# Kernel tuning notes

Hardware: AMD Instinct MI355X
Metric: run time of the kernel (lower is better)

## Reference

```python
import jax, jax.numpy as jnp
import numpy as np
import math

N, E, B, T = 100000, 500000, 4096, 12
IN, HID, H = 64, 32, 4
HC = HID * H  # 128
ED = 4


def setup_inputs() -> dict:
    key = jax.random.key(0)
    ks = jax.random.split(key, 40)
    w = lambda k, shape: jax.random.normal(k, shape, jnp.float32) * 0.05
    inp = {
        'x': jax.random.normal(ks[0], (N, IN), jnp.float32),
        'edge_index': jax.random.randint(ks[1], (2, E), 0, N, jnp.int32),
        'edge_attr': jax.random.normal(ks[2], (E, ED), jnp.float32),
        'batch': jnp.sort(jax.random.randint(ks[3], (N,), 0, B, jnp.int32)),
        'r_target': jax.random.randint(ks[4], (B,), 0, T, jnp.int32),
        # layer 1 (in=IN)
        'Wq1': w(ks[5], (IN, HC)), 'bq1': w(ks[6], (HC,)),
        'Wk1': w(ks[7], (IN, HC)), 'bk1': w(ks[8], (HC,)),
        'Wv1': w(ks[9], (IN, HC)), 'bv1': w(ks[10], (HC,)),
        'We1': w(ks[11], (ED, HC)),
        'Ws1': w(ks[12], (IN, HC)), 'bs1': w(ks[13], (HC,)),
        # layers 2 and 3 stacked (in=HC)
        'Wq23': w(ks[14], (2, HC, HC)), 'bq23': w(ks[15], (2, HC)),
        'Wk23': w(ks[16], (2, HC, HC)), 'bk23': w(ks[17], (2, HC)),
        'Wv23': w(ks[18], (2, HC, HC)), 'bv23': w(ks[19], (2, HC)),
        'We23': w(ks[20], (2, ED, HC)),
        'Ws23': w(ks[21], (2, HC, HC)), 'bs23': w(ks[22], (2, HC)),
        # per-task linear heads (out_channels=1)
        'head_W': w(ks[23], (T, HC)), 'head_b': w(ks[24], (T,)),
    }
    return inp


def tconv(x, src, dst, ea, Wq, bq, Wk, bk, Wv, bv, We, Ws, bs):
    """PyG TransformerConv: gather -> per-edge MHA score -> segment softmax -> scatter."""
    q = (x @ Wq + bq).reshape(-1, H, HID)   # [N,H,C]
    k = (x @ Wk + bk).reshape(-1, H, HID)
    v = (x @ Wv + bv).reshape(-1, H, HID)
    e = (ea @ We).reshape(-1, H, HID)       # [E,H,C] (lin_edge has no bias)
    kj = k[src] + e                          # [E,H,C]
    alpha = (q[dst] * kj).sum(-1) / math.sqrt(HID)          # [E,H]
    amax = jax.ops.segment_max(alpha, dst, num_segments=N)  # [N,H]
    alpha = jnp.exp(alpha - amax[dst])
    asum = jax.ops.segment_sum(alpha, dst, num_segments=N)
    alpha = alpha / (asum[dst] + 1e-16)
    msg = (v[src] + e) * alpha[..., None]                   # [E,H,C]
    out = jax.ops.segment_sum(msg, dst, num_segments=N).reshape(N, HC)
    return out + x @ Ws + bs                 # root_weight skip connection


def reference(x, edge_index, edge_attr, batch, r_target,
              Wq1, bq1, Wk1, bk1, Wv1, bv1, We1, Ws1, bs1,
              Wq23, bq23, Wk23, bk23, Wv23, bv23, We23, Ws23, bs23,
              head_W, head_b):
    src, dst = edge_index[0], edge_index[1]
    h = jax.nn.relu(tconv(x, src, dst, edge_attr, Wq1, bq1, Wk1, bk1, Wv1, bv1, We1, Ws1, bs1))
    h = jax.nn.relu(tconv(h, src, dst, edge_attr, Wq23[0], bq23[0], Wk23[0], bk23[0], Wv23[0], bv23[0], We23[0], Ws23[0], bs23[0]))
    h = tconv(h, src, dst, edge_attr, Wq23[1], bq23[1], Wk23[1], bk23[1], Wv23[1], bv23[1], We23[1], Ws23[1], bs23[1])
    # global mean pool per graph
    cnt = jax.ops.segment_sum(jnp.ones((N,), h.dtype), batch, num_segments=B)
    pooled = jax.ops.segment_sum(h, batch, num_segments=B) / jnp.maximum(cnt, 1.0)[:, None]  # [B,HC]
    # dropout p=0.3 is a no-op in eval mode
    # per-task head selected by r_target (out_channels=1, squeezed)
    return (pooled * head_W[r_target]).sum(-1) + head_b[r_target]  # [B]
```

## Files before the change

### kernel.cpp

```cpp
#include <hip/hip_runtime.h>
#include <hip/hip_bf16.h>

#define NN 100000
#define EE 500000
#define BB 4096
#define HC 128
#define SCAN_ELEM 1024
#define NSB ((NN + SCAN_ELEM - 1) / SCAN_ELEM)

typedef __bf16 bf16_t;
typedef bf16_t bf16x8 __attribute__((ext_vector_type(8)));
typedef float f32x4 __attribute__((ext_vector_type(4)));
typedef float f32x2 __attribute__((ext_vector_type(2)));

__device__ __forceinline__ unsigned short f2bf(float f) {
    unsigned u = __builtin_bit_cast(unsigned, f);
    u += 0x7FFFu + ((u >> 16) & 1u);
    return (unsigned short)(u >> 16);
}
__device__ __forceinline__ float bflo(unsigned u) {
    return __builtin_bit_cast(float, u << 16);
}
__device__ __forceinline__ float bfhi(unsigned u) {
    return __builtin_bit_cast(float, u & 0xFFFF0000u);
}
__device__ __forceinline__ f32x2 unpk2(unsigned u) {
    return (f32x2){ bflo(u), bfhi(u) };
}

__global__ __launch_bounds__(256) void prep_w(
    const float* __restrict__ Wq, const float* __restrict__ Wk,
    const float* __restrict__ Wv, const float* __restrict__ Ws,
    unsigned short* __restrict__ Wt, int K)
{
    const int g = blockIdx.x * 256 + threadIdx.x;
    const int per = K * 128;
    if (g >= 4 * per) return;
    const int p = g / per, r = g - p * per;
    const int k = r >> 7, n = r & 127;
    const float* W = p == 0 ? Wq : p == 1 ? Wk : p == 2 ? Wv : Ws;
    Wt[(size_t)p * per + (size_t)n * K + k] = f2bf(W[k * 128 + n]);
}

template<int NKT, int F32A>
__global__ __launch_bounds__(256) void gemm_mfma(
    const unsigned short* __restrict__ Abf,
    const float* __restrict__ xf,
    const unsigned short* __restrict__ Wt,
    const float* __restrict__ bq, const float* __restrict__ bk,
    const float* __restrict__ bv, const float* __restrict__ bs,
    unsigned* __restrict__ QSb, unsigned* __restrict__ KVb)
{
    constexpr int K = NKT * 32;
    const int lane = threadIdx.x & 63;
    const int p = threadIdx.x >> 6;
    const int m = lane & 15, kq = lane >> 4;
    const int rows0 = blockIdx.x * 32;

    const unsigned short* Wp = Wt + (size_t)p * 128 * K;
    const float* bias = p == 0 ? bq : p == 1 ? bk : p == 2 ? bv : bs;

    bf16x8 a[2][NKT];
#pragma unroll
    for (int mt = 0; mt < 2; mt++)
#pragma unroll
        for (int kt = 0; kt < NKT; kt++) {
            if constexpr (F32A) {
                const float* pr = xf + (size_t)(rows0 + mt * 16 + m) * K + kt * 32 + kq * 8;
                const float4 f0 = *(const float4*)pr;
                const float4 f1 = *(const float4*)(pr + 4);
                union { bf16x8 v; unsigned short u8[8]; } cv;
                cv.u8[0] = f2bf(f0.x); cv.u8[1] = f2bf(f0.y);
                cv.u8[2] = f2bf(f0.z); cv.u8[3] = f2bf(f0.w);
                cv.u8[4] = f2bf(f1.x); cv.u8[5] = f2bf(f1.y);
                cv.u8[6] = f2bf(f1.z); cv.u8[7] = f2bf(f1.w);
                a[mt][kt] = cv.v;
            } else {
                a[mt][kt] = *(const bf16x8*)(Abf + (size_t)(rows0 + mt * 16 + m) * K + kt * 32 + kq * 8);
            }
        }

    f32x4 acc[2][8];
#pragma unroll
    for (int mt = 0; mt < 2; mt++)
#pragma unroll
        for (int nt = 0; nt < 8; nt++)
            acc[mt][nt] = (f32x4){0.f, 0.f, 0.f, 0.f};

#pragma unroll
    for (int nt = 0; nt < 8; nt++) {
#pragma unroll
        for (int kt = 0; kt < NKT; kt++) {
            const bf16x8 b = *(const bf16x8*)(Wp + (size_t)(nt * 16 + m) * K + kt * 32 + kq * 8);
            acc[0][nt] = __builtin_amdgcn_mfma_f32_16x16x32_bf16(a[0][kt], b, acc[0][nt], 0, 0, 0);
            acc[1][nt] = __builtin_amdgcn_mfma_f32_16x16x32_bf16(a[1][kt], b, acc[1][nt], 0, 0, 0);
        }
    }

    unsigned* out = p == 0 ? QSb : p == 1 ? KVb : p == 2 ? (KVb + 64) : (QSb + 64);
#pragma unroll
    for (int nt = 0; nt < 8; nt++) {
        const float bi = bias[nt * 16 + m];
#pragma unroll
        for (int mt = 0; mt < 2; mt++) {
#pragma unroll
            for (int r = 0; r < 4; r++) {
                const float v0 = acc[mt][nt][r] + bi;
                const float v1 = __shfl_xor(v0, 1);
                if (!(m & 1)) {
                    const unsigned pk = (unsigned)f2bf(v0) | ((unsigned)f2bf(v1) << 16);
                    out[(size_t)(rows0 + mt * 16 + kq * 4 + r) * 128 + nt * 8 + (m >> 1)] = pk;
                }
            }
        }
    }
}

__global__ __launch_bounds__(256) void deg_k(const int* __restrict__ ei, int* __restrict__ deg)
{
    const int e = blockIdx.x * 256 + threadIdx.x;
    if (e < EE) atomicAdd(&deg[ei[EE + e]], 1);
}

__global__ __launch_bounds__(256) void scan_part(const int* __restrict__ deg,
                                                 int* __restrict__ bsum)
{
    __shared__ int red[256];
    const int base = blockIdx.x * SCAN_ELEM + threadIdx.x * 4;
    int s = 0;
#pragma unroll
    for (int j = 0; j < 4; j++) { const int i = base + j; if (i < NN) s += deg[i]; }
    red[threadIdx.x] = s;
    __syncthreads();
    for (int st = 128; st > 0; st >>= 1) {
        if (threadIdx.x < st) red[threadIdx.x] += red[threadIdx.x + st];
        __syncthreads();
    }
    if (threadIdx.x == 0) bsum[blockIdx.x] = red[0];
}

__global__ __launch_bounds__(128) void scan_top(const int* __restrict__ bsum,
                                                int* __restrict__ boff)
{
    __shared__ int buf[128];
    const int v = (threadIdx.x < NSB) ? bsum[threadIdx.x] : 0;
    buf[threadIdx.x] = v;
    __syncthreads();
    for (int s = 1; s < 128; s <<= 1) {
        const int t = (threadIdx.x >= s) ? buf[threadIdx.x - s] : 0;
        __syncthreads();
        buf[threadIdx.x] += t;
        __syncthreads();
    }
    if (threadIdx.x < NSB) boff[threadIdx.x] = buf[threadIdx.x] - v;
}

__global__ __launch_bounds__(256) void scan_final(const int* __restrict__ deg,
                                                  const int* __restrict__ boff,
                                                  int* __restrict__ off,
                                                  int* __restrict__ cursor)
{
    __shared__ int tsum[256];
    const int base = blockIdx.x * SCAN_ELEM + threadIdx.x * 4;
    int vals[4];
    int s = 0;
#pragma unroll
    for (int j = 0; j < 4; j++) {
        const int i = base + j;
        vals[j] = (i < NN) ? deg[i] : 0;
        s += vals[j];
    }
    tsum[threadIdx.x] = s;
    __syncthreads();
    for (int st = 1; st < 256; st <<= 1) {
        const int t = (threadIdx.x >= st) ? tsum[threadIdx.x - st] : 0;
        __syncthreads();
        tsum[threadIdx.x] += t;
        __syncthreads();
    }
    int ex = boff[blockIdx.x] + tsum[threadIdx.x] - s;
#pragma unroll
    for (int j = 0; j < 4; j++) {
        const int i = base + j;
        if (i < NN) { off[i] = ex; cursor[i] = ex; }
        ex += vals[j];
    }
    if (blockIdx.x == NSB - 1 && threadIdx.x == 255)
        off[NN] = boff[blockIdx.x] + tsum[255];
}

__global__ __launch_bounds__(256) void bucket_k(const int* __restrict__ ei,
                                                const float* __restrict__ ea,
                                                int* __restrict__ cursor,
                                                int* __restrict__ esrc,
                                                float4* __restrict__ eaf)
{
    const int e = blockIdx.x * 256 + threadIdx.x;
    if (e < EE) {
        const int d = ei[EE + e];
        const int p = atomicAdd(&cursor[d], 1);
        esrc[p] = ei[e];
        eaf[p] = *(const float4*)(ea + (size_t)e * 4);
    }
}

__global__ __launch_bounds__(256) void cnt_k(const int* __restrict__ batch,
                                             float* __restrict__ cnt)
{
    const int n = blockIdx.x * 256 + threadIdx.x;
    if (n < NN) atomicAdd(&cnt[batch[n]], 1.0f);
}

__global__ __launch_bounds__(256) void edge_fused(
    const int* __restrict__ esrc, const float4* __restrict__ eaf,
    const float* __restrict__ We,
    const unsigned* __restrict__ QSb, const unsigned* __restrict__ KVb,
    const int* __restrict__ off,
    unsigned short* __restrict__ Hb,
    const int* __restrict__ batch, float* __restrict__ pooled,
    int fuse_pool)
{
    const int lane = threadIdx.x & 63;
    const int slot = lane >> 4;
    const int c8   = lane & 15;
    const int cb   = c8 * 8;
    const int ceq  = cb + slot * 2;
    const int n = blockIdx.x * 4 + (threadIdx.x >> 6);

    const int beg = off[n], end = off[n + 1];

    const uint4 qv = *(const uint4*)(QSb + (size_t)n * 128 + c8 * 4);
    const unsigned sku = QSb[(size_t)n * 128 + 64 + c8 * 4 + slot];
    f32x2 q2[4];
    q2[0] = unpk2(qv.x); q2[1] = unpk2(qv.y);
    q2[2] = unpk2(qv.z); q2[3] = unpk2(qv.w);

    float qep[4];
#pragma unroll
    for (int d = 0; d < 4; d++) {
        const float4 wa = *(const float4*)(We + d * HC + cb);
        const float4 wb = *(const float4*)(We + d * HC + cb + 4);
        qep[d] = wa.x * q2[0].x + wa.y * q2[0].y + wa.z * q2[1].x + wa.w * q2[1].y
               + wb.x * q2[2].x + wb.y * q2[2].y + wb.z * q2[3].x + wb.w * q2[3].y;
    }

    f32x2 num2[4] = {(f32x2){0.f, 0.f}, (f32x2){0.f, 0.f},
                     (f32x2){0.f, 0.f}, (f32x2){0.f, 0.f}};
    f32x4 s4 = (f32x4){0.f, 0.f, 0.f, 0.f};
    float den = 0.f;

    if (beg < end) {
        const int e1 = end - 1;
        int p0 = beg + slot; if (p0 > e1) p0 = e1;
        int src = esrc[p0];
        float4 a4 = eaf[p0];
        for (int base = beg; base < end; base += 4) {
            const unsigned* kv = KVb + (size_t)src * 128 + c8 * 4;
            const uint4 ku = *(const uint4*)kv;
            const uint4 vu = *(const uint4*)(kv + 64);
            const float4 ac = a4;
            const bool act = (base + slot) < end;
            if (base + 4 < end) {
                int pn = base + 4 + slot; if (pn > e1) pn = e1;
                src = esrc[pn]; a4 = eaf[pn];
            }
            f32x2 t2 = q2[0] * unpk2(ku.x);
            t2 += q2[1] * unpk2(ku.y);
            t2 += q2[2] * unpk2(ku.z);
            t2 += q2[3] * unpk2(ku.w);
            float tot = t2.x + t2.y
                      + ac.x * qep[0] + ac.y * qep[1] + ac.z * qep[2] + ac.w * qep[3];
            tot += __shfl_xor(tot, 1);
            tot += __shfl_xor(tot, 2);
            float al = __expf(tot * 0.17677669529663687f);
            if (!act) al = 0.f;
            num2[0] += unpk2(vu.x) * al;
            num2[1] += unpk2(vu.y) * al;
            num2[2] += unpk2(vu.z) * al;
            num2[3] += unpk2(vu.w) * al;
            s4.x += ac.x * al; s4.y += ac.y * al;
            s4.z += ac.z * al; s4.w += ac.w * al;
            den += al;
        }
    }

#pragma unroll
    for (int j = 0; j < 4; j++) {
        num2[j].x += __shfl_xor(num2[j].x, 16);
        num2[j].y += __shfl_xor(num2[j].y, 16);
        num2[j].x += __shfl_xor(num2[j].x, 32);
        num2[j].y += __shfl_xor(num2[j].y, 32);
    }
    s4.x += __shfl_xor(s4.x, 16); s4.y += __shfl_xor(s4.y, 16);
    s4.z += __shfl_xor(s4.z, 16); s4.w += __shfl_xor(s4.w, 16);
    s4.x += __shfl_xor(s4.x, 32); s4.y += __shfl_xor(s4.y, 32);
    s4.z += __shfl_xor(s4.z, 32); s4.w += __shfl_xor(s4.w, 32);
    den += __shfl_xor(den, 16);
    den += __shfl_xor(den, 32);
    const float inv = 1.f / (den + 1e-16f);

    f32x2 mynum = slot == 0 ? num2[0] : slot == 1 ? num2[1]
                : slot == 2 ? num2[2] : num2[3];
    float ev0 = 0.f, ev1 = 0.f;
#pragma unroll
    for (int d = 0; d < 4; d++) {
        const float2 wd = *(const float2*)(We + d * HC + ceq);
        const float sd = d == 0 ? s4.x : d == 1 ? s4.y : d == 2 ? s4.z : s4.w;
        ev0 += sd * wd.x;
        ev1 += sd * wd.y;
    }
    const float o0 = (mynum.x + ev0) * inv + bflo(sku);
    const float o1 = (mynum.y + ev1) * inv + bfhi(sku);

    if (!fuse_pool) {
        const float r0 = fmaxf(o0, 0.f), r1 = fmaxf(o1, 0.f);
        const unsigned pk = (unsigned)f2bf(r0) | ((unsigned)f2bf(r1) << 16);
        *(unsigned*)(Hb + (size_t)n * HC + ceq) = pk;
    } else {
        const int b = batch[n];
        atomicAdd(pooled + (size_t)b * HC + ceq,     o0);
        atomicAdd(pooled + (size_t)b * HC + ceq + 1, o1);
    }
}

__global__ __launch_bounds__(256) void head_k(
    const float* __restrict__ pooled, const float* __restrict__ cnt,
    const int* __restrict__ rt, const float* __restrict__ hW,
    const float* __restrict__ hb, float* __restrict__ out)
{
    const int lane = threadIdx.x & 63;
    const int b = blockIdx.x * 4 + (threadIdx.x >> 6);
    if (b >= BB) return;
    const int t = rt[b];
    const int c = lane * 2;
    const float2 p2 = *(const float2*)(pooled + (size_t)b * HC + c);
    const float2 w2 = *(const float2*)(hW + (size_t)t * HC + c);
    float part = p2.x * w2.x + p2.y * w2.y;
    part += __shfl_xor(part, 1);
    part += __shfl_xor(part, 2);
    part += __shfl_xor(part, 4);
    part += __shfl_xor(part, 8);
    part += __shfl_xor(part, 16);
    part += __shfl_xor(part, 32);
    if (lane == 0) out[b] = part / fmaxf(cnt[b], 1.0f) + hb[t];
}

extern "C" void kernel_launch(void* const* d_in, const int* in_sizes, int n_in,
                              void* d_out, int out_size, void* d_ws, size_t ws_size,
                              hipStream_t stream) {
    const float* x      = (const float*)d_in[0];
    const int*   ei     = (const int*)d_in[1];
    const float* ea     = (const float*)d_in[2];
    const int*   batch  = (const int*)d_in[3];
    const int*   rt     = (const int*)d_in[4];

    unsigned* QSb = (unsigned*)d_ws;
    unsigned* KVb = QSb + 12800000;
    unsigned short* Abf = (unsigned short*)(KVb + 12800000);
    float4* eaf   = (float4*)(Abf + 12800000);
    unsigned short* Wt = (unsigned short*)(eaf + 500000);
    float* pooled = (float*)(Wt + 65536);
    float* cnt    = pooled + 524288;
    int*   esrc   = (int*)(cnt + 4096);
    int*   deg    = esrc + 500000;
    int*   off    = deg + 100000;
    int*   cursor = off + 100004;
    int*   bsum   = cursor + 100000;
    int*   boff   = bsum + 128;

    hipMemsetAsync(deg, 0, 100000 * sizeof(int), stream);
    deg_k<<<(EE + 255) / 256, 256, 0, stream>>>(ei, deg);
    scan_part<<<NSB, 256, 0, stream>>>(deg, bsum);
    scan_top<<<1, 128, 0, stream>>>(bsum, boff);
    scan_final<<<NSB, 256, 0, stream>>>(deg, boff, off, cursor);
    bucket_k<<<(EE + 255) / 256, 256, 0, stream>>>(ei, ea, cursor, esrc, eaf);

    hipMemsetAsync(pooled, 0, (size_t)(BB * HC + BB) * sizeof(float), stream);
    cnt_k<<<(NN + 255) / 256, 256, 0, stream>>>(batch, cnt);

    for (int l = 0; l < 3; l++) {
        const int K = (l == 0) ? 64 : 128;
        const float *Wq, *Wk, *Wv, *Wsk, *bq, *bk, *bv, *bs, *We;
        if (l == 0) {
            Wq = (const float*)d_in[5];  bq = (const float*)d_in[6];
            Wk = (const float*)d_in[7];  bk = (const float*)d_in[8];
            Wv = (const float*)d_in[9];  bv = (const float*)d_in[10];
            We = (const float*)d_in[11];
            Wsk= (const float*)d_in[12]; bs = (const float*)d_in[13];
        } else {
            const int j = l - 1;
            Wq = (const float*)d_in[14] + (size_t)j * HC * HC;  bq = (const float*)d_in[15] + j * HC;
            Wk = (const float*)d_in[16] + (size_t)j * HC * HC;  bk = (const float*)d_in[17] + j * HC;
            Wv = (const float*)d_in[18] + (size_t)j * HC * HC;  bv = (const float*)d_in[19] + j * HC;
            We = (const float*)d_in[20] + (size_t)j * 4 * HC;
            Wsk= (const float*)d_in[21] + (size_t)j * HC * HC;  bs = (const float*)d_in[22] + j * HC;
        }

        prep_w<<<(4 * K * 128 + 255) / 256, 256, 0, stream>>>(Wq, Wk, Wv, Wsk, Wt, K);
        if (K == 64)
            gemm_mfma<2, 1><<<NN / 32, 256, 0, stream>>>(Abf, x, Wt, bq, bk, bv, bs, QSb, KVb);
        else
            gemm_mfma<4, 0><<<NN / 32, 256, 0, stream>>>(Abf, x, Wt, bq, bk, bv, bs, QSb, KVb);
        edge_fused<<<NN / 4, 256, 0, stream>>>(esrc, eaf, We, QSb, KVb, off,
                                               Abf, batch, pooled,
                                               l == 2 ? 1 : 0);
    }

    head_k<<<BB / 4, 256, 0, stream>>>(pooled, cnt, rt,
        (const float*)d_in[23], (const float*)d_in[24], (float*)d_out);
}
```

Before: 664.6 us.

## Process eight edges per wave iteration with sixteen channels per lane

Remaps the per-node wave so each lane covers 16 channels (two heads' worth across a lane pair) and 8 edge slots run concurrently instead of 4. This halves the loop trip count per node and issues more independent gathers in flight, which targets latency on low-degree nodes (average degree is about 5). In exchange it doubles per-lane registers for q, num and loaded K/V, makes the cross-slot reduction longer (three shuffle stages over more values), and leaves more slots idle on nodes with few edges.

```diff
diff --git a/kernel.cpp b/kernel.cpp
--- a/kernel.cpp
+++ b/kernel.cpp
@@ -221,31 +221,39 @@
     int fuse_pool)
 {
     const int lane = threadIdx.x & 63;
-    const int slot = lane >> 4;
-    const int c8   = lane & 15;
-    const int cb   = c8 * 8;
+    const int slot = lane >> 3;
+    const int c8   = lane & 7;
+    const int cb   = c8 * 16;
     const int ceq  = cb + slot * 2;
     const int n = blockIdx.x * 4 + (threadIdx.x >> 6);
 
-    const int beg = off[n], end = off[n + 1];
-
-    const uint4 qv = *(const uint4*)(QSb + (size_t)n * 128 + c8 * 4);
-    const unsigned sku = QSb[(size_t)n * 128 + 64 + c8 * 4 + slot];
-    f32x2 q2[4];
-    q2[0] = unpk2(qv.x); q2[1] = unpk2(qv.y);
-    q2[2] = unpk2(qv.z); q2[3] = unpk2(qv.w);
+    const int2 be = *(const int2*)(off + n);
+    const int beg = be.x, end = be.y;
+
+    const uint4 qva = *(const uint4*)(QSb + (size_t)n * 128 + c8 * 8);
+    const uint4 qvb = *(const uint4*)(QSb + (size_t)n * 128 + c8 * 8 + 4);
+    const unsigned sku = QSb[(size_t)n * 128 + 64 + c8 * 8 + slot];
+    f32x2 q2[8];
+    q2[0] = unpk2(qva.x); q2[1] = unpk2(qva.y);
+    q2[2] = unpk2(qva.z); q2[3] = unpk2(qva.w);
+    q2[4] = unpk2(qvb.x); q2[5] = unpk2(qvb.y);
+    q2[6] = unpk2(qvb.z); q2[7] = unpk2(qvb.w);
 
     float qep[4];
 #pragma unroll
     for (int d = 0; d < 4; d++) {
-        const float4 wa = *(const float4*)(We + d * HC + cb);
-        const float4 wb = *(const float4*)(We + d * HC + cb + 4);
-        qep[d] = wa.x * q2[0].x + wa.y * q2[0].y + wa.z * q2[1].x + wa.w * q2[1].y
-               + wb.x * q2[2].x + wb.y * q2[2].y + wb.z * q2[3].x + wb.w * q2[3].y;
-    }
-
-    f32x2 num2[4] = {(f32x2){0.f, 0.f}, (f32x2){0.f, 0.f},
-                     (f32x2){0.f, 0.f}, (f32x2){0.f, 0.f}};
+        float acc = 0.f;
+#pragma unroll
+        for (int j = 0; j < 4; j++) {
+            const float4 w4 = *(const float4*)(We + d * HC + cb + j * 4);
+            acc += w4.x * q2[2 * j].x + w4.y * q2[2 * j].y
+                 + w4.z * q2[2 * j + 1].x + w4.w * q2[2 * j + 1].y;
+        }
+        qep[d] = acc;
+    }
+
+    f32x2 num2[8] = {(f32x2){0.f,0.f},(f32x2){0.f,0.f},(f32x2){0.f,0.f},(f32x2){0.f,0.f},
+                     (f32x2){0.f,0.f},(f32x2){0.f,0.f},(f32x2){0.f,0.f},(f32x2){0.f,0.f}};
     f32x4 s4 = (f32x4){0.f, 0.f, 0.f, 0.f};
     float den = 0.f;
 
@@ -254,30 +262,39 @@
         int p0 = beg + slot; if (p0 > e1) p0 = e1;
         int src = esrc[p0];
         float4 a4 = eaf[p0];
-        for (int base = beg; base < end; base += 4) {
-            const unsigned* kv = KVb + (size_t)src * 128 + c8 * 4;
-            const uint4 ku = *(const uint4*)kv;
-            const uint4 vu = *(const uint4*)(kv + 64);
+        for (int base = beg; base < end; base += 8) {
+            const unsigned* kv = KVb + (size_t)src * 128 + c8 * 8;
+            const uint4 ka = *(const uint4*)kv;
+            const uint4 kb = *(const uint4*)(kv + 4);
+            const uint4 va = *(const uint4*)(kv + 64);
+            const uint4 vb = *(const uint4*)(kv + 68);
             const float4 ac = a4;
             const bool act = (base + slot) < end;
-            if (base + 4 < end) {
-                int pn = base + 4 + slot; if (pn > e1) pn = e1;
+            if (base + 8 < end) {
+                int pn = base + 8 + slot; if (pn > e1) pn = e1;
                 src = esrc[pn]; a4 = eaf[pn];
             }
-            f32x2 t2 = q2[0] * unpk2(ku.x);
-            t2 += q2[1] * unpk2(ku.y);
-            t2 += q2[2] * unpk2(ku.z);
-            t2 += q2[3] * unpk2(ku.w);
+            f32x2 t2 = q2[0] * unpk2(ka.x);
+            t2 += q2[1] * unpk2(ka.y);
+            t2 += q2[2] * unpk2(ka.z);
+            t2 += q2[3] * unpk2(ka.w);
+            t2 += q2[4] * unpk2(kb.x);
+            t2 += q2[5] * unpk2(kb.y);
+            t2 += q2[6] * unpk2(kb.z);
+            t2 += q2[7] * unpk2(kb.w);
             float tot = t2.x + t2.y
                       + ac.x * qep[0] + ac.y * qep[1] + ac.z * qep[2] + ac.w * qep[3];
             tot += __shfl_xor(tot, 1);
-            tot += __shfl_xor(tot, 2);
             float al = __expf(tot * 0.17677669529663687f);
             if (!act) al = 0.f;
-            num2[0] += unpk2(vu.x) * al;
-            num2[1] += unpk2(vu.y) * al;
-            num2[2] += unpk2(vu.z) * al;
-            num2[3] += unpk2(vu.w) * al;
+            num2[0] += unpk2(va.x) * al;
+            num2[1] += unpk2(va.y) * al;
+            num2[2] += unpk2(va.z) * al;
+            num2[3] += unpk2(va.w) * al;
+            num2[4] += unpk2(vb.x) * al;
+            num2[5] += unpk2(vb.y) * al;
+            num2[6] += unpk2(vb.z) * al;
+            num2[7] += unpk2(vb.w) * al;
             s4.x += ac.x * al; s4.y += ac.y * al;
             s4.z += ac.z * al; s4.w += ac.w * al;
             den += al;
@@ -285,22 +302,29 @@
     }
 
 #pragma unroll
-    for (int j = 0; j < 4; j++) {
-        num2[j].x += __shfl_xor(num2[j].x, 16);
-        num2[j].y += __shfl_xor(num2[j].y, 16);
-        num2[j].x += __shfl_xor(num2[j].x, 32);
-        num2[j].y += __shfl_xor(num2[j].y, 32);
-    }
-    s4.x += __shfl_xor(s4.x, 16); s4.y += __shfl_xor(s4.y, 16);
-    s4.z += __shfl_xor(s4.z, 16); s4.w += __shfl_xor(s4.w, 16);
-    s4.x += __shfl_xor(s4.x, 32); s4.y += __shfl_xor(s4.y, 32);
-    s4.z += __shfl_xor(s4.z, 32); s4.w += __shfl_xor(s4.w, 32);
-    den += __shfl_xor(den, 16);
-    den += __shfl_xor(den, 32);
+    for (int st = 8; st < 64; st <<= 1) {
+#pragma unroll
+        for (int j = 0; j < 8; j++) {
+            num2[j].x += __shfl_xor(num2[j].x, st);
+            num2[j].y += __shfl_xor(num2[j].y, st);
+        }
+        s4.x += __shfl_xor(s4.x, st); s4.y += __shfl_xor(s4.y, st);
+        s4.z += __shfl_xor(s4.z, st); s4.w += __shfl_xor(s4.w, st);
+        den += __shfl_xor(den, st);
+    }
     const float inv = 1.f / (den + 1e-16f);
 
-    f32x2 mynum = slot == 0 ? num2[0] : slot == 1 ? num2[1]
-                : slot == 2 ? num2[2] : num2[3];
+    f32x2 mynum;
+    switch (slot) {
+        case 0: mynum = num2[0]; break;
+        case 1: mynum = num2[1]; break;
+        case 2: mynum = num2[2]; break;
+        case 3: mynum = num2[3]; break;
+        case 4: mynum = num2[4]; break;
+        case 5: mynum = num2[5]; break;
+        case 6: mynum = num2[6]; break;
+        default: mynum = num2[7]; break;
+    }
     float ev0 = 0.f, ev1 = 0.f;
 #pragma unroll
     for (int d = 0; d < 4; d++) {
```

After: 899.6 us. +35.4%, slower.

## Process two destination nodes per wavefront in edge kernel, fold cnt into scan

Applied to the files above, without the earlier changes.

The edge attention kernel now assigns two adjacent destination nodes to each 64-lane wavefront and interleaves their gathers and softmax accumulation. This halves the grid and aims to expose more independent memory loads per wave, hiding the latency of random K/V gathers. The separate graph-count kernel is removed and its atomics are folded into scan_final, saving one launch. The cost is higher register pressure and some divergence when the two nodes have different degrees.

```diff
diff --git a/kernel.cpp b/kernel.cpp
--- a/kernel.cpp
+++ b/kernel.cpp
@@ -158,7 +158,9 @@
 __global__ __launch_bounds__(256) void scan_final(const int* __restrict__ deg,
                                                   const int* __restrict__ boff,
                                                   int* __restrict__ off,
-                                                  int* __restrict__ cursor)
+                                                  int* __restrict__ cursor,
+                                                  const int* __restrict__ batch,
+                                                  float* __restrict__ cnt)
 {
     __shared__ int tsum[256];
     const int base = blockIdx.x * SCAN_ELEM + threadIdx.x * 4;
@@ -182,7 +184,10 @@
 #pragma unroll
     for (int j = 0; j < 4; j++) {
         const int i = base + j;
-        if (i < NN) { off[i] = ex; cursor[i] = ex; }
+        if (i < NN) {
+            off[i] = ex; cursor[i] = ex;
+            atomicAdd(&cnt[batch[i]], 1.0f);
+        }
         ex += vals[j];
     }
     if (blockIdx.x == NSB - 1 && threadIdx.x == 255)
@@ -202,13 +207,6 @@
         esrc[p] = ei[e];
         eaf[p] = *(const float4*)(ea + (size_t)e * 4);
     }
-}
-
-__global__ __launch_bounds__(256) void cnt_k(const int* __restrict__ batch,
-                                             float* __restrict__ cnt)
-{
-    const int n = blockIdx.x * 256 + threadIdx.x;
-    if (n < NN) atomicAdd(&cnt[batch[n]], 1.0f);
 }
 
 __global__ __launch_bounds__(256) void edge_fused(
@@ -225,101 +223,162 @@
     const int c8   = lane & 15;
     const int cb   = c8 * 8;
     const int ceq  = cb + slot * 2;
-    const int n = blockIdx.x * 4 + (threadIdx.x >> 6);
-
-    const int beg = off[n], end = off[n + 1];
-
-    const uint4 qv = *(const uint4*)(QSb + (size_t)n * 128 + c8 * 4);
-    const unsigned sku = QSb[(size_t)n * 128 + 64 + c8 * 4 + slot];
-    f32x2 q2[4];
-    q2[0] = unpk2(qv.x); q2[1] = unpk2(qv.y);
-    q2[2] = unpk2(qv.z); q2[3] = unpk2(qv.w);
-
-    float qep[4];
+    const int nA = (blockIdx.x * 4 + (threadIdx.x >> 6)) * 2;
+    const int nB = nA + 1;
+
+    const int2 beA = *(const int2*)(off + nA);
+    const int begA = beA.x, endA = beA.y;
+    const int begB = endA, endB = off[nB + 1];
+    const int dA = endA - begA, dB = endB - begB;
+
+    const uint4 qvA = *(const uint4*)(QSb + (size_t)nA * 128 + c8 * 4);
+    const uint4 qvB = *(const uint4*)(QSb + (size_t)nB * 128 + c8 * 4);
+    const unsigned skA = QSb[(size_t)nA * 128 + 64 + c8 * 4 + slot];
+    const unsigned skB = QSb[(size_t)nB * 128 + 64 + c8 * 4 + slot];
+    f32x2 qA[4], qB[4];
+    qA[0] = unpk2(qvA.x); qA[1] = unpk2(qvA.y);
+    qA[2] = unpk2(qvA.z); qA[3] = unpk2(qvA.w);
+    qB[0] = unpk2(qvB.x); qB[1] = unpk2(qvB.y);
+    qB[2] = unpk2(qvB.z); qB[3] = unpk2(qvB.w);
+
+    float qepA[4], qepB[4];
 #pragma unroll
     for (int d = 0; d < 4; d++) {
         const float4 wa = *(const float4*)(We + d * HC + cb);
         const float4 wb = *(const float4*)(We + d * HC + cb + 4);
-        qep[d] = wa.x * q2[0].x + wa.y * q2[0].y + wa.z * q2[1].x + wa.w * q2[1].y
-               + wb.x * q2[2].x + wb.y * q2[2].y + wb.z * q2[3].x + wb.w * q2[3].y;
-    }
-
-    f32x2 num2[4] = {(f32x2){0.f, 0.f}, (f32x2){0.f, 0.f},
-                     (f32x2){0.f, 0.f}, (f32x2){0.f, 0.f}};
-    f32x4 s4 = (f32x4){0.f, 0.f, 0.f, 0.f};
-    float den = 0.f;
-
-    if (beg < end) {
-        const int e1 = end - 1;
-        int p0 = beg + slot; if (p0 > e1) p0 = e1;
-        int src = esrc[p0];
-        float4 a4 = eaf[p0];
-        for (int base = beg; base < end; base += 4) {
-            const unsigned* kv = KVb + (size_t)src * 128 + c8 * 4;
-            const uint4 ku = *(const uint4*)kv;
-            const uint4 vu = *(const uint4*)(kv + 64);
-            const float4 ac = a4;
-            const bool act = (base + slot) < end;
-            if (base + 4 < end) {
-                int pn = base + 4 + slot; if (pn > e1) pn = e1;
-                src = esrc[pn]; a4 = eaf[pn];
+        qepA[d] = wa.x * qA[0].x + wa.y * qA[0].y + wa.z * qA[1].x + wa.w * qA[1].y
+                + wb.x * qA[2].x + wb.y * qA[2].y + wb.z * qA[3].x + wb.w * qA[3].y;
+        qepB[d] = wa.x * qB[0].x + wa.y * qB[0].y + wa.z * qB[1].x + wa.w * qB[1].y
+                + wb.x * qB[2].x + wb.y * qB[2].y + wb.z * qB[3].x + wb.w * qB[3].y;
+    }
+
+    f32x2 numA[4] = {(f32x2){0.f,0.f},(f32x2){0.f,0.f},(f32x2){0.f,0.f},(f32x2){0.f,0.f}};
+    f32x2 numB[4] = {(f32x2){0.f,0.f},(f32x2){0.f,0.f},(f32x2){0.f,0.f},(f32x2){0.f,0.f}};
+    f32x4 s4A = (f32x4){0.f,0.f,0.f,0.f}, s4B = (f32x4){0.f,0.f,0.f,0.f};
+    float denA = 0.f, denB = 0.f;
+
+    int srcA = 0, srcB = 0;
+    float4 a4A = make_float4(0.f,0.f,0.f,0.f), a4B = make_float4(0.f,0.f,0.f,0.f);
+    if (dA > 0) { const int p = begA + (slot < dA ? slot : dA - 1); srcA = esrc[p]; a4A = eaf[p]; }
+    if (dB > 0) { const int p = begB + (slot < dB ? slot : dB - 1); srcB = esrc[p]; a4B = eaf[p]; }
+
+    const int dmax = dA > dB ? dA : dB;
+    for (int o = 0; o < dmax; o += 4) {
+        const bool anyA = o < dA, anyB = o < dB;
+        uint4 kuA, vuA, kuB, vuB;
+        float4 acA, acB;
+        if (anyA) {
+            const unsigned* kv = KVb + (size_t)srcA * 128 + c8 * 4;
+            kuA = *(const uint4*)kv; vuA = *(const uint4*)(kv + 64);
+        }
+        if (anyB) {
+            const unsigned* kv = KVb + (size_t)srcB * 128 + c8 * 4;
+            kuB = *(const uint4*)kv; vuB = *(const uint4*)(kv + 64);
+        }
+        if (anyA) {
+            acA = a4A;
+            if (o + 4 < dA) {
+                const int t = o + 4 + slot;
+                const int p = begA + (t < dA ? t : dA - 1);
+                srcA = esrc[p]; a4A = eaf[p];
             }
-            f32x2 t2 = q2[0] * unpk2(ku.x);
-            t2 += q2[1] * unpk2(ku.y);
-            t2 += q2[2] * unpk2(ku.z);
-            t2 += q2[3] * unpk2(ku.w);
+        }
+        if (anyB) {
+            acB = a4B;
+            if (o + 4 < dB) {
+                const int t = o + 4 + slot;
+                const int p = begB + (t < dB ? t : dB - 1);
+                srcB = esrc[p]; a4B = eaf[p];
+            }
+        }
+        if (anyA) {
+            f32x2 t2 = qA[0] * unpk2(kuA.x);
+            t2 += qA[1] * unpk2(kuA.y);
+            t2 += qA[2] * unpk2(kuA.z);
+            t2 += qA[3] * unpk2(kuA.w);
             float tot = t2.x + t2.y
-                      + ac.x * qep[0] + ac.y * qep[1] + ac.z * qep[2] + ac.w * qep[3];
+                      + acA.x * qepA[0] + acA.y * qepA[1] + acA.z * qepA[2] + acA.w * qepA[3];
             tot += __shfl_xor(tot, 1);
             tot += __shfl_xor(tot, 2);
             float al = __expf(tot * 0.17677669529663687f);
-            if (!act) al = 0.f;
-            num2[0] += unpk2(vu.x) * al;
-            num2[1] += unpk2(vu.y) * al;
-            num2[2] += unpk2(vu.z) * al;
-            num2[3] += unpk2(vu.w) * al;
-            s4.x += ac.x * al; s4.y += ac.y * al;
-            s4.z += ac.z * al; s4.w += ac.w * al;
-            den += al;
-        }
-    }
-
-#pragma unroll
-    for (int j = 0; j < 4; j++) {
-        num2[j].x += __shfl_xor(num2[j].x, 16);
-        num2[j].y += __shfl_xor(num2[j].y, 16);
-        num2[j].x += __shfl_xor(num2[j].x, 32);
-        num2[j].y += __shfl_xor(num2[j].y, 32);
-    }
-    s4.x += __shfl_xor(s4.x, 16); s4.y += __shfl_xor(s4.y, 16);
-    s4.z += __shfl_xor(s4.z, 16); s4.w += __shfl_xor(s4.w, 16);
-    s4.x += __shfl_xor(s4.x, 32); s4.y += __shfl_xor(s4.y, 32);
-    s4.z += __shfl_xor(s4.z, 32); s4.w += __shfl_xor(s4.w, 32);
-    den += __shfl_xor(den, 16);
-    den += __shfl_xor(den, 32);
-    const float inv = 1.f / (den + 1e-16f);
-
-    f32x2 mynum = slot == 0 ? num2[0] : slot == 1 ? num2[1]
-                : slot == 2 ? num2[2] : num2[3];
-    float ev0 = 0.f, ev1 = 0.f;
+            if ((o + slot) >= dA) al = 0.f;
+            numA[0] += unpk2(vuA.x) * al;
+            numA[1] += unpk2(vuA.y) * al;
+            numA[2] += unpk2(vuA.z) * al;
+            numA[3] += unpk2(vuA.w) * al;
+            s4A.x += acA.x * al; s4A.y += acA.y * al;
+            s4A.z += acA.z * al; s4A.w += acA.w * al;
+            denA += al;
+        }
+        if (anyB) {
+            f32x2 t2 = qB[0] * unpk2(kuB.x);
+            t2 += qB[1] * unpk2(kuB.y);
+            t2 += qB[2] * unpk2(kuB.z);
+            t2 += qB[3] * unpk2(kuB.w);
+            float tot = t2.x + t2.y
+                      + acB.x * qepB[0] + acB.y * qepB[1] + acB.z * qepB[2] + acB.w * qepB[3];
+            tot += __shfl_xor(tot, 1);
+            tot += __shfl_xor(tot, 2);
+            float al = __expf(tot * 0.17677669529663687f);
+            if ((o + slot) >= dB) al = 0.f;
+            numB[0] += unpk2(vuB.x) * al;
+            numB[1] += unpk2(vuB.y) * al;
+            numB[2] += unpk2(vuB.z) * al;
+            numB[3] += unpk2(vuB.w) * al;
+            s4B.x += acB.x * al; s4B.y += acB.y * al;
+            s4B.z += acB.z * al; s4B.w += acB.w * al;
+            denB += al;
+        }
+    }
+
+#pragma unroll
+    for (int st = 16; st < 64; st <<= 1) {
+#pragma unroll
+        for (int j = 0; j < 4; j++) {
+            numA[j].x += __shfl_xor(numA[j].x, st);
+            numA[j].y += __shfl_xor(numA[j].y, st);
+            numB[j].x += __shfl_xor(numB[j].x, st);
+            numB[j].y += __shfl_xor(numB[j].y, st);
+        }
+        s4A.x += __shfl_xor(s4A.x, st); s4A.y += __shfl_xor(s4A.y, st);
+        s4A.z += __shfl_xor(s4A.z, st); s4A.w += __shfl_xor(s4A.w, st);
+        s4B.x += __shfl_xor(s4B.x, st); s4B.y += __shfl_xor(s4B.y, st);
+        s4B.z += __shfl_xor(s4B.z, st); s4B.w += __shfl_xor(s4B.w, st);
+        denA += __shfl_xor(denA, st);
+        denB += __shfl_xor(denB, st);
+    }
+    const float invA = 1.f / (denA + 1e-16f);
+    const float invB = 1.f / (denB + 1e-16f);
+
+    f32x2 mynA = slot == 0 ? numA[0] : slot == 1 ? numA[1]
+               : slot == 2 ? numA[2] : numA[3];
+    f32x2 mynB = slot == 0 ? numB[0] : slot == 1 ? numB[1]
+               : slot == 2 ? numB[2] : numB[3];
+    float evA0 = 0.f, evA1 = 0.f, evB0 = 0.f, evB1 = 0.f;
 #pragma unroll
     for (int d = 0; d < 4; d++) {
         const float2 wd = *(const float2*)(We + d * HC + ceq);
-        const float sd = d == 0 ? s4.x : d == 1 ? s4.y : d == 2 ? s4.z : s4.w;
-        ev0 += sd * wd.x;
-        ev1 += sd * wd.y;
-    }
-    const float o0 = (mynum.x + ev0) * inv + bflo(sku);
-    const float o1 = (mynum.y + ev1) * inv + bfhi(sku);
+        const float sdA = d == 0 ? s4A.x : d == 1 ? s4A.y : d == 2 ? s4A.z : s4A.w;
+        const float sdB = d == 0 ? s4B.x : d == 1 ? s4B.y : d == 2 ? s4B.z : s4B.w;
+        evA0 += sdA * wd.x; evA1 += sdA * wd.y;
+        evB0 += sdB * wd.x; evB1 += sdB * wd.y;
+    }
+    const float oA0 = (mynA.x + evA0) * invA + bflo(skA);
+    const float oA1 = (mynA.y + evA1) * invA + bfhi(skA);
+    const float oB0 = (mynB.x + evB0) * invB + bflo(skB);
+    const float oB1 = (mynB.y + evB1) * invB + bfhi(skB);
 
     if (!fuse_pool) {
-        const float r0 = fmaxf(o0, 0.f), r1 = fmaxf(o1, 0.f);
-        const unsigned pk = (unsigned)f2bf(r0) | ((unsigned)f2bf(r1) << 16);
-        *(unsigned*)(Hb + (size_t)n * HC + ceq) = pk;
+        const unsigned pkA = (unsigned)f2bf(fmaxf(oA0, 0.f)) | ((unsigned)f2bf(fmaxf(oA1, 0.f)) << 16);
+        const unsigned pkB = (unsigned)f2bf(fmaxf(oB0, 0.f)) | ((unsigned)f2bf(fmaxf(oB1, 0.f)) << 16);
+        *(unsigned*)(Hb + (size_t)nA * HC + ceq) = pkA;
+        *(unsigned*)(Hb + (size_t)nB * HC + ceq) = pkB;
     } else {
-        const int b = batch[n];
-        atomicAdd(pooled + (size_t)b * HC + ceq,     o0);
-        atomicAdd(pooled + (size_t)b * HC + ceq + 1, o1);
+        const int bA = batch[nA], bB = batch[nB];
+        atomicAdd(pooled + (size_t)bA * HC + ceq,     oA0);
+        atomicAdd(pooled + (size_t)bA * HC + ceq + 1, oA1);
+        atomicAdd(pooled + (size_t)bB * HC + ceq,     oB0);
+        atomicAdd(pooled + (size_t)bB * HC + ceq + 1, oB1);
     }
 }
 
@@ -369,14 +428,12 @@
     int*   boff   = bsum + 128;
 
     hipMemsetAsync(deg, 0, 100000 * sizeof(int), stream);
+    hipMemsetAsync(pooled, 0, (size_t)(BB * HC + BB) * sizeof(float), stream);
     deg_k<<<(EE + 255) / 256, 256, 0, stream>>>(ei, deg);
     scan_part<<<NSB, 256, 0, stream>>>(deg, bsum);
     scan_top<<<1, 128, 0, stream>>>(bsum, boff);
-    scan_final<<<NSB, 256, 0, stream>>>(deg, boff, off, cursor);
+    scan_final<<<NSB, 256, 0, stream>>>(deg, boff, off, cursor, batch, cnt);
     bucket_k<<<(EE + 255) / 256, 256, 0, stream>>>(ei, ea, cursor, esrc, eaf);
-
-    hipMemsetAsync(pooled, 0, (size_t)(BB * HC + BB) * sizeof(float), stream);
-    cnt_k<<<(NN + 255) / 256, 256, 0, stream>>>(batch, cnt);
 
     for (int l = 0; l < 3; l++) {
         const int K = (l == 0) ? 64 : 128;
@@ -401,7 +458,7 @@
             gemm_mfma<2, 1><<<NN / 32, 256, 0, stream>>>(Abf, x, Wt, bq, bk, bv, bs, QSb, KVb);
         else
             gemm_mfma<4, 0><<<NN / 32, 256, 0, stream>>>(Abf, x, Wt, bq, bk, bv, bs, QSb, KVb);
-        edge_fused<<<NN / 4, 256, 0, stream>>>(esrc, eaf, We, QSb, KVb, off,
+        edge_fused<<<NN / 8, 256, 0, stream>>>(esrc, eaf, We, QSb, KVb, off,
                                                Abf, batch, pooled,
                                                l == 2 ? 1 : 0);
     }
```

Result: slower. 693.4 us (+4.3%).
